# Optimization experiments

Hardware: AMD Instinct MI355X
Metric: run time of the kernel (lower is better)

## Reference

```python
import jax, jax.numpy as jnp
import numpy as np

D_MODEL = 1024
D_FF = 4 * D_MODEL
NUM_EXPERTS = 8
TOP_K = 2
TOKENS = 4096


def setup_inputs() -> dict:
    key = jax.random.key(0)
    ks = jax.random.split(key, 8)
    s = 0.02
    x = jax.random.normal(ks[0], (TOKENS, D_MODEL), dtype=jnp.float32)
    Wg = jax.random.normal(ks[1], (D_MODEL, NUM_EXPERTS), dtype=jnp.float32) * s
    bg = jnp.zeros((NUM_EXPERTS,), dtype=jnp.float32)
    W1 = jax.random.normal(ks[2], (NUM_EXPERTS, D_MODEL, D_FF), dtype=jnp.float32) * s
    b1 = jnp.zeros((NUM_EXPERTS, D_FF), dtype=jnp.float32)
    W2 = jax.random.normal(ks[3], (NUM_EXPERTS, D_FF, D_MODEL), dtype=jnp.float32) * s
    b2 = jnp.zeros((NUM_EXPERTS, D_MODEL), dtype=jnp.float32)
    return {"x": x, "Wg": Wg, "bg": bg, "W1": W1, "b1": b1, "W2": W2, "b2": b2}


def reference(x, Wg, bg, W1, b1, W2, b2):
    # Gating: softmax over experts, select top-k indices per token.
    gate_scores = jax.nn.softmax(x @ Wg + bg, axis=-1)        # [T, E]
    _, top_k_idx = jax.lax.top_k(gate_scores, TOP_K)          # [T, K]
    # Binary combine mask: 1 where expert selected (top_k indices are distinct).
    # NOTE: original sums selected expert outputs WITHOUT gate weighting.
    mask = jnp.sum(jax.nn.one_hot(top_k_idx, NUM_EXPERTS, dtype=x.dtype), axis=1)  # [T, E]
    out = jnp.zeros_like(x)
    for e in range(NUM_EXPERTS):  # small fixed expert count
        h = jax.nn.relu(x @ W1[e] + b1[e])                    # [T, 4D]
        y = h @ W2[e] + b2[e]                                 # [T, D]
        out = out + mask[:, e:e + 1] * y
    return out
```

## Files before the change

kernel.cpp:

```cpp
#include <hip/hip_runtime.h>
#include <hip/hip_bf16.h>

#define T_TOKENS 4096
#define DM 1024
#define DF 4096
#define NE 8
#define MAXROWS 9216

typedef float f32x4 __attribute__((ext_vector_type(4)));
typedef short bf16x8 __attribute__((ext_vector_type(8)));

__device__ __forceinline__ unsigned short f2bf(float f) {
    union { float f; unsigned int u; } v; v.f = f;
    unsigned int r = v.u + 0x7fffu + ((v.u >> 16) & 1u);
    return (unsigned short)(r >> 16);
}

__device__ __forceinline__ void g2l16(const void* g, void* l) {
    __builtin_amdgcn_global_load_lds(
        (const __attribute__((address_space(1))) void*)g,
        (__attribute__((address_space(3))) void*)l, 16, 0, 0);
}

__global__ __launch_bounds__(256) void gate_kernel(
    const float* __restrict__ x, const float* __restrict__ Wg, const float* __restrict__ bg,
    int* __restrict__ counts, int* __restrict__ topk, unsigned short* __restrict__ xb)
{
    int wave = threadIdx.x >> 6;
    int lane = threadIdx.x & 63;
    int t = blockIdx.x * 4 + wave;
    float acc[NE];
#pragma unroll
    for (int e = 0; e < NE; e++) acc[e] = 0.f;
    const float* xr = x + (size_t)t * DM;
    unsigned short* xbr = xb + (size_t)t * DM;
#pragma unroll
    for (int i = 0; i < DM / 64; i++) {
        int d = lane + i * 64;
        float xv = xr[d];
        xbr[d] = f2bf(xv);
        const float4* wg = (const float4*)(Wg + d * NE);
        float4 w0 = wg[0], w1 = wg[1];
        acc[0] += xv * w0.x; acc[1] += xv * w0.y; acc[2] += xv * w0.z; acc[3] += xv * w0.w;
        acc[4] += xv * w1.x; acc[5] += xv * w1.y; acc[6] += xv * w1.z; acc[7] += xv * w1.w;
    }
#pragma unroll
    for (int e = 0; e < NE; e++) {
#pragma unroll
        for (int off = 32; off > 0; off >>= 1)
            acc[e] += __shfl_down(acc[e], off);
    }
    if (lane == 0) {
        float lg[NE];
#pragma unroll
        for (int e = 0; e < NE; e++) lg[e] = acc[e] + bg[e];
        int b1i = 0; float b1v = lg[0];
        for (int e = 1; e < NE; e++) if (lg[e] > b1v) { b1v = lg[e]; b1i = e; }
        int b2i = -1; float b2v = -1e30f;
        for (int e = 0; e < NE; e++) {
            if (e == b1i) continue;
            if (b2i < 0 || lg[e] > b2v) { b2v = lg[e]; b2i = e; }
        }
        topk[t * 2 + 0] = b1i;
        topk[t * 2 + 1] = b2i;
        atomicAdd(&counts[b1i], 1);
        atomicAdd(&counts[b2i], 1);
    }
}

__global__ __launch_bounds__(256) void scatter_kernel(
    const int* __restrict__ counts, const int* __restrict__ topk,
    int* __restrict__ offsets, int* __restrict__ list)
{
    __shared__ int offs[NE + 1];
    __shared__ int cur[NE];
    if (threadIdx.x == 0) {
        int s = 0;
        for (int e = 0; e < NE; e++) {
            offs[e] = s; offsets[e] = s;
            s += (counts[e] + 127) & ~127;
        }
        offs[NE] = s; offsets[NE] = s;
    }
    if (threadIdx.x < NE) cur[threadIdx.x] = 0;
    __syncthreads();
    for (int i = threadIdx.x; i < T_TOKENS * 2; i += 256) {
        int e = topk[i];
        int pos = atomicAdd(&cur[e], 1);
        list[offs[e] + pos] = i >> 1;
    }
    __syncthreads();
    for (int e = 0; e < NE; e++) {
        int s = offs[e] + counts[e];
        int t = offs[e + 1];
        for (int i = s + threadIdx.x; i < t; i += 256) list[i] = -1;
    }
}

__global__ __launch_bounds__(256) void tr_cvt_kernel(
    const float* __restrict__ src, unsigned short* __restrict__ dst, int K, int N)
{
    const int e = blockIdx.z;
    src += (size_t)e * K * N;
    dst += (size_t)e * N * K;
    const int n0 = blockIdx.x * 64, k0 = blockIdx.y * 256;
    __shared__ unsigned short tile[64][264];
    const int t = threadIdx.x;
    const int c4 = (t & 15) * 4;
    const int kr = t >> 4;
#pragma unroll
    for (int r = 0; r < 16; r++) {
        int k = kr + r * 16;
        float4 v = *(const float4*)(src + (size_t)(k0 + k) * N + n0 + c4);
        tile[c4 + 0][k] = f2bf(v.x);
        tile[c4 + 1][k] = f2bf(v.y);
        tile[c4 + 2][k] = f2bf(v.z);
        tile[c4 + 3][k] = f2bf(v.w);
    }
    __syncthreads();
    const int rg = t >> 5;
    const int c = t & 31;
#pragma unroll
    for (int r = 0; r < 8; r++) {
        int n = rg + r * 8;
        *(uint4*)(dst + (size_t)(n0 + n) * K + k0 + c * 8) = *(const uint4*)&tile[n][c * 8];
    }
}

__global__ __launch_bounds__(256) void gemm1_kernel(
    const unsigned short* __restrict__ xb, const unsigned short* __restrict__ W1T,
    const float* __restrict__ b1, const int* __restrict__ offsets,
    const int* __restrict__ list, unsigned short* __restrict__ H)
{
    const int bid = blockIdx.x;
    const int W = (bid & 7) * 288 + (bid >> 3);
    const int bx = W >> 5;
    const int by = W & 31;

    const int total = offsets[NE];
    const int row0 = bx * 128;
    if (row0 >= total) return;
    int e = 0;
    while (row0 >= offsets[e + 1]) e++;
    const int n0 = by * 128;

    __shared__ unsigned short Asm[128 * 32];
    __shared__ unsigned short Bsm[128 * 32];

    const int tid = threadIdx.x;
    const int w = tid >> 6, lane = tid & 63;
    const int quad = lane >> 4, l16 = lane & 15;
    const int wm = w >> 1, wn = w & 1;

    const int sr = lane >> 2;
    const int sc = (((lane & 3) ^ ((sr >> 1) & 3))) * 8;
    const int qx8 = (quad ^ ((l16 >> 1) & 3)) * 8;

    const int ra1 = 32 * w + sr, ra2 = ra1 + 16;
    int t1 = list[row0 + ra1]; if (t1 < 0) t1 = 0;
    int t2 = list[row0 + ra2]; if (t2 < 0) t2 = 0;
    const unsigned short* gA1 = xb + (size_t)t1 * DM + sc;
    const unsigned short* gA2 = xb + (size_t)t2 * DM + sc;
    const unsigned short* Wb = W1T + (size_t)e * DF * DM;
    const unsigned short* gB1 = Wb + (size_t)(n0 + 32 * w + sr) * DM + sc;
    const unsigned short* gB2 = gB1 + (size_t)16 * DM;
    unsigned short* lA1 = Asm + (2 * w) * 512;
    unsigned short* lA2 = Asm + (2 * w + 1) * 512;
    unsigned short* lB1 = Bsm + (2 * w) * 512;
    unsigned short* lB2 = Bsm + (2 * w + 1) * 512;

    f32x4 acc[4][4];
#pragma unroll
    for (int i = 0; i < 4; i++)
#pragma unroll
        for (int j = 0; j < 4; j++) acc[i][j] = (f32x4){0.f, 0.f, 0.f, 0.f};

    for (int kk = 0; kk < DM; kk += 32) {
        g2l16(gA1 + kk, lA1);
        g2l16(gA2 + kk, lA2);
        g2l16(gB1 + kk, lB1);
        g2l16(gB2 + kk, lB2);
        __syncthreads();
        bf16x8 af[4];
#pragma unroll
        for (int i = 0; i < 4; i++)
            af[i] = *(const bf16x8*)&Asm[(wm * 64 + i * 16 + l16) * 32 + qx8];
#pragma unroll
        for (int j = 0; j < 4; j++) {
            bf16x8 bfv = *(const bf16x8*)&Bsm[(wn * 64 + j * 16 + l16) * 32 + qx8];
#pragma unroll
            for (int i = 0; i < 4; i++)
                acc[i][j] = __builtin_amdgcn_mfma_f32_16x16x32_bf16(af[i], bfv, acc[i][j], 0, 0, 0);
        }
        __syncthreads();
    }

    const float* bias = b1 + e * DF;
#pragma unroll
    for (int j = 0; j < 4; j++) {
        int n = n0 + wn * 64 + j * 16 + l16;
        float bj = bias[n];
#pragma unroll
        for (int i = 0; i < 4; i++) {
            int row = row0 + wm * 64 + i * 16 + quad * 4;
#pragma unroll
            for (int r = 0; r < 4; r++) {
                float v = acc[i][j][r] + bj;
                v = fmaxf(v, 0.f);
                H[(size_t)(row + r) * DF + n] = f2bf(v);
            }
        }
    }
}

__global__ __launch_bounds__(256) void gemm2_kernel(
    const unsigned short* __restrict__ H, const unsigned short* __restrict__ W2T,
    const float* __restrict__ b2, const int* __restrict__ offsets,
    const int* __restrict__ list, float* __restrict__ out)
{
    const int bid = blockIdx.x;
    const int W = (bid & 7) * 72 + (bid >> 3);
    const int bx = W >> 3;
    const int by = W & 7;

    const int total = offsets[NE];
    const int row0 = bx * 128;
    if (row0 >= total) return;
    int e = 0;
    while (row0 >= offsets[e + 1]) e++;
    const int n0 = by * 128;

    __shared__ unsigned short Asm[128 * 32];
    __shared__ unsigned short Bsm[128 * 32];

    const int tid = threadIdx.x;
    const int w = tid >> 6, lane = tid & 63;
    const int quad = lane >> 4, l16 = lane & 15;
    const int wm = w >> 1, wn = w & 1;

    const int sr = lane >> 2;
    const int sc = (((lane & 3) ^ ((sr >> 1) & 3))) * 8;
    const int qx8 = (quad ^ ((l16 >> 1) & 3)) * 8;

    const unsigned short* gA1 = H + (size_t)(row0 + 32 * w + sr) * DF + sc;
    const unsigned short* gA2 = gA1 + (size_t)16 * DF;
    const unsigned short* Wb = W2T + (size_t)e * DM * DF;
    const unsigned short* gB1 = Wb + (size_t)(n0 + 32 * w + sr) * DF + sc;
    const unsigned short* gB2 = gB1 + (size_t)16 * DF;
    unsigned short* lA1 = Asm + (2 * w) * 512;
    unsigned short* lA2 = Asm + (2 * w + 1) * 512;
    unsigned short* lB1 = Bsm + (2 * w) * 512;
    unsigned short* lB2 = Bsm + (2 * w + 1) * 512;

    f32x4 acc[4][4];
#pragma unroll
    for (int i = 0; i < 4; i++)
#pragma unroll
        for (int j = 0; j < 4; j++) acc[i][j] = (f32x4){0.f, 0.f, 0.f, 0.f};

    for (int kk = 0; kk < DF; kk += 32) {
        g2l16(gA1 + kk, lA1);
        g2l16(gA2 + kk, lA2);
        g2l16(gB1 + kk, lB1);
        g2l16(gB2 + kk, lB2);
        __syncthreads();
        bf16x8 af[4];
#pragma unroll
        for (int i = 0; i < 4; i++)
            af[i] = *(const bf16x8*)&Asm[(wm * 64 + i * 16 + l16) * 32 + qx8];
#pragma unroll
        for (int j = 0; j < 4; j++) {
            bf16x8 bfv = *(const bf16x8*)&Bsm[(wn * 64 + j * 16 + l16) * 32 + qx8];
#pragma unroll
            for (int i = 0; i < 4; i++)
                acc[i][j] = __builtin_amdgcn_mfma_f32_16x16x32_bf16(af[i], bfv, acc[i][j], 0, 0, 0);
        }
        __syncthreads();
    }

    const float* bias = b2 + e * DM;
#pragma unroll
    for (int j = 0; j < 4; j++) {
        int n = n0 + wn * 64 + j * 16 + l16;
        float bj = bias[n];
#pragma unroll
        for (int i = 0; i < 4; i++) {
            int row = row0 + wm * 64 + i * 16 + quad * 4;
#pragma unroll
            for (int r = 0; r < 4; r++) {
                int tk = list[row + r];
                if (tk >= 0)
                    atomicAdd(&out[(size_t)tk * DM + n], acc[i][j][r] + bj);
            }
        }
    }
}

extern "C" void kernel_launch(void* const* d_in, const int* in_sizes, int n_in,
                              void* d_out, int out_size, void* d_ws, size_t ws_size,
                              hipStream_t stream)
{
    const float* x  = (const float*)d_in[0];
    const float* Wg = (const float*)d_in[1];
    const float* bg = (const float*)d_in[2];
    const float* W1 = (const float*)d_in[3];
    const float* b1 = (const float*)d_in[4];
    const float* W2 = (const float*)d_in[5];
    const float* b2 = (const float*)d_in[6];
    float* out = (float*)d_out;

    char* ws = (char*)d_ws;
    int* counts  = (int*)(ws + 0);
    int* offsets = (int*)(ws + 64);
    int* topk    = (int*)(ws + 256);
    int* list    = (int*)(ws + 33024);
    unsigned short* xb = (unsigned short*)(ws + (1u << 20));
    unsigned short* WT = (unsigned short*)(ws + (16u << 20));
    unsigned short* Hb = (unsigned short*)(ws + (80u << 20));

    hipMemsetAsync(counts, 0, NE * sizeof(int), stream);
    hipMemsetAsync(d_out, 0, (size_t)out_size * sizeof(float), stream);

    gate_kernel<<<T_TOKENS / 4, 256, 0, stream>>>(x, Wg, bg, counts, topk, xb);
    scatter_kernel<<<1, 256, 0, stream>>>(counts, topk, offsets, list);

    tr_cvt_kernel<<<dim3(DF / 64, DM / 256, NE), 256, 0, stream>>>(W1, WT, DM, DF);
    gemm1_kernel<<<dim3((MAXROWS / 128) * (DF / 128)), 256, 0, stream>>>(
        xb, WT, b1, offsets, list, Hb);

    tr_cvt_kernel<<<dim3(DM / 64, DF / 256, NE), 256, 0, stream>>>(W2, WT, DF, DM);
    gemm2_kernel<<<dim3((MAXROWS / 128) * (DM / 128)), 256, 0, stream>>>(
        Hb, WT, b2, offsets, list, out);
}
```

Before: 664.4 us.

## Pre-tile transposed bf16 weights into swizzled LDS-ready 32x32 blocks

The weight transpose-convert kernel now writes the bf16 weights in a tiled layout: 32-column by 32-k blocks, already in the XOR-swizzled order the GEMM's LDS tile expects. Each wave's B load in gemm1 and gemm2 becomes one contiguous 1 KB chunk per k-step instead of 16 strided rows. This is meant to improve global-load coalescing and DRAM/TLB locality for the weight stream. The converter's own access pattern changes: strided LDS reads and 4 chunks per block, which may shift its cost.

```diff
diff --git a/kernel.cpp b/kernel.cpp
--- a/kernel.cpp
+++ b/kernel.cpp
@@ -97,33 +97,51 @@
     }
 }
 
-__global__ __launch_bounds__(256) void tr_cvt_kernel(
+__global__ __launch_bounds__(256) void tr_cvt_tiled_kernel(
     const float* __restrict__ src, unsigned short* __restrict__ dst, int K, int N)
 {
     const int e = blockIdx.z;
     src += (size_t)e * K * N;
     dst += (size_t)e * N * K;
-    const int n0 = blockIdx.x * 64, k0 = blockIdx.y * 256;
-    __shared__ unsigned short tile[64][264];
+    const int k0 = blockIdx.y * 32;
+    const int k32 = blockIdx.y;
+    const int nslab = blockIdx.x * 1024;
+    const int K32 = K >> 5;
+
+    __shared__ unsigned short tl[32][264];
+
     const int t = threadIdx.x;
-    const int c4 = (t & 15) * 4;
-    const int kr = t >> 4;
-#pragma unroll
-    for (int r = 0; r < 16; r++) {
-        int k = kr + r * 16;
-        float4 v = *(const float4*)(src + (size_t)(k0 + k) * N + n0 + c4);
-        tile[c4 + 0][k] = f2bf(v.x);
-        tile[c4 + 1][k] = f2bf(v.y);
-        tile[c4 + 2][k] = f2bf(v.z);
-        tile[c4 + 3][k] = f2bf(v.w);
-    }
-    __syncthreads();
-    const int rg = t >> 5;
-    const int c = t & 31;
-#pragma unroll
-    for (int r = 0; r < 8; r++) {
-        int n = rg + r * 8;
-        *(uint4*)(dst + (size_t)(n0 + n) * K + k0 + c * 8) = *(const uint4*)&tile[n][c * 8];
+    const int rquart = t >> 6;
+    const int col4 = (t & 63) * 4;
+    const int g = t >> 5;
+    const int q = t & 31;
+    const int kg = (q & 3) ^ (((q >> 2) >> 1) & 3);
+
+    for (int c = 0; c < 4; c++) {
+        const int nbase = nslab + c * 256;
+#pragma unroll
+        for (int rr = 0; rr < 8; rr++) {
+            int row = rr * 4 + rquart;
+            float4 v = *(const float4*)(src + (size_t)(k0 + row) * N + nbase + col4);
+            unsigned short o[4] = { f2bf(v.x), f2bf(v.y), f2bf(v.z), f2bf(v.w) };
+            *(uint2*)&tl[row][col4] = *(const uint2*)o;
+        }
+        __syncthreads();
+        const int n32 = (nbase >> 5) + g;
+        unsigned short* dt = dst + ((size_t)n32 * K32 + k32) * 1024;
+#pragma unroll
+        for (int h = 0; h < 2; h++) {
+#pragma unroll
+            for (int p = 0; p < 2; p++) {
+                int l = q + 32 * p;
+                int nr = 32 * g + 16 * h + (l >> 2);
+                unsigned short tmp[8];
+#pragma unroll
+                for (int j = 0; j < 8; j++) tmp[j] = tl[8 * kg + j][nr];
+                *(uint4*)(dt + h * 512 + l * 8) = *(const uint4*)tmp;
+            }
+        }
+        __syncthreads();
     }
 }
 
@@ -161,9 +179,8 @@
     int t2 = list[row0 + ra2]; if (t2 < 0) t2 = 0;
     const unsigned short* gA1 = xb + (size_t)t1 * DM + sc;
     const unsigned short* gA2 = xb + (size_t)t2 * DM + sc;
-    const unsigned short* Wb = W1T + (size_t)e * DF * DM;
-    const unsigned short* gB1 = Wb + (size_t)(n0 + 32 * w + sr) * DM + sc;
-    const unsigned short* gB2 = gB1 + (size_t)16 * DM;
+    const unsigned short* gB1 = W1T + (size_t)e * DF * DM
+        + ((size_t)(n0 / 32 + w) * (DM / 32)) * 1024 + lane * 8;
     unsigned short* lA1 = Asm + (2 * w) * 512;
     unsigned short* lA2 = Asm + (2 * w + 1) * 512;
     unsigned short* lB1 = Bsm + (2 * w) * 512;
@@ -178,8 +195,8 @@
     for (int kk = 0; kk < DM; kk += 32) {
         g2l16(gA1 + kk, lA1);
         g2l16(gA2 + kk, lA2);
-        g2l16(gB1 + kk, lB1);
-        g2l16(gB2 + kk, lB2);
+        g2l16(gB1 + kk * 32, lB1);
+        g2l16(gB1 + kk * 32 + 512, lB2);
         __syncthreads();
         bf16x8 af[4];
 #pragma unroll
@@ -244,9 +261,8 @@
 
     const unsigned short* gA1 = H + (size_t)(row0 + 32 * w + sr) * DF + sc;
     const unsigned short* gA2 = gA1 + (size_t)16 * DF;
-    const unsigned short* Wb = W2T + (size_t)e * DM * DF;
-    const unsigned short* gB1 = Wb + (size_t)(n0 + 32 * w + sr) * DF + sc;
-    const unsigned short* gB2 = gB1 + (size_t)16 * DF;
+    const unsigned short* gB1 = W2T + (size_t)e * DM * DF
+        + ((size_t)(n0 / 32 + w) * (DF / 32)) * 1024 + lane * 8;
     unsigned short* lA1 = Asm + (2 * w) * 512;
     unsigned short* lA2 = Asm + (2 * w + 1) * 512;
     unsigned short* lB1 = Bsm + (2 * w) * 512;
@@ -261,8 +277,8 @@
     for (int kk = 0; kk < DF; kk += 32) {
         g2l16(gA1 + kk, lA1);
         g2l16(gA2 + kk, lA2);
-        g2l16(gB1 + kk, lB1);
-        g2l16(gB2 + kk, lB2);
+        g2l16(gB1 + kk * 32, lB1);
+        g2l16(gB1 + kk * 32 + 512, lB2);
         __syncthreads();
         bf16x8 af[4];
 #pragma unroll
@@ -324,11 +340,11 @@
     gate_kernel<<<T_TOKENS / 4, 256, 0, stream>>>(x, Wg, bg, counts, topk, xb);
     scatter_kernel<<<1, 256, 0, stream>>>(counts, topk, offsets, list);
 
-    tr_cvt_kernel<<<dim3(DF / 64, DM / 256, NE), 256, 0, stream>>>(W1, WT, DM, DF);
+    tr_cvt_tiled_kernel<<<dim3(DF / 1024, DM / 32, NE), 256, 0, stream>>>(W1, WT, DM, DF);
     gemm1_kernel<<<dim3((MAXROWS / 128) * (DF / 128)), 256, 0, stream>>>(
         xb, WT, b1, offsets, list, Hb);
 
-    tr_cvt_kernel<<<dim3(DM / 64, DF / 256, NE), 256, 0, stream>>>(W2, WT, DF, DM);
+    tr_cvt_tiled_kernel<<<dim3(DM / 1024, DF / 32, NE), 256, 0, stream>>>(W2, WT, DF, DM);
     gemm2_kernel<<<dim3((MAXROWS / 128) * (DM / 128)), 256, 0, stream>>>(
         Hb, WT, b2, offsets, list, out);
 }
```

New measurement: 656.9 us. No clear change (-1.1%).
